# Optimization experiments

Hardware: AMD Instinct MI355X
Metric: run time of the kernel (lower is better)

## Reference

```python
import jax, jax.numpy as jnp
import numpy as np

RES = 64  # fixed roi_map resolution (replaces per-ROI ceil(width)/ceil(height) dynamic sizes for jit)
SMOOTH_L1_BETA = 1.0 / 9.0


def setup_inputs() -> dict:
    key = jax.random.key(0)
    ks = jax.random.split(key, 8)
    N, C = 4096, 91
    R, K, HM = 1024, 17, 56
    class_logits = jax.random.normal(ks[0], (N, C), dtype=jnp.float32)
    box_regression = jax.random.normal(ks[1], (N, C * 4), dtype=jnp.float32)
    labels = jax.random.randint(ks[2], (N,), 0, C, dtype=jnp.int32)
    regression_targets = jax.random.normal(ks[3], (N, 4), dtype=jnp.float32)
    kp_maps = jax.random.normal(ks[4], (R, K, HM, HM), dtype=jnp.float32)
    xy = jax.random.uniform(ks[5], (R, 2), dtype=jnp.float32) * 512.0
    wh = 32.0 + jax.random.uniform(ks[6], (R, 2), dtype=jnp.float32) * 256.0
    kp_rois = jnp.concatenate([xy, xy + wh], axis=1)  # valid xyxy boxes
    mask_logits = jax.random.normal(ks[7], (R, C, 28, 28), dtype=jnp.float32)
    mask_labels = jax.random.randint(jax.random.fold_in(key, 9), (R,), 0, C, dtype=jnp.int32)
    return {
        "class_logits": class_logits,
        "box_regression": box_regression,
        "labels": labels,
        "regression_targets": regression_targets,
        "kp_maps": kp_maps,
        "kp_rois": kp_rois,
        "mask_logits": mask_logits,
        "mask_labels": mask_labels,
    }


def _fastrcnn_loss(class_logits, box_regression, labels, regression_targets):
    N, C = class_logits.shape
    # classification: mean cross entropy
    logp = jax.nn.log_softmax(class_logits, axis=-1)
    cls_loss = -jnp.take_along_axis(logp, labels[:, None], axis=1)[:, 0].mean()
    br = box_regression.reshape(N, C, 4)
    sel = jnp.take_along_axis(br, labels[:, None, None].astype(jnp.int32) * jnp.ones((1, 1, 4), jnp.int32), axis=1)[:, 0]  # [N,4]
    d = sel - regression_targets
    ad = jnp.abs(d)
    sl1 = jnp.where(ad < SMOOTH_L1_BETA, 0.5 * d * d / SMOOTH_L1_BETA, ad - 0.5 * SMOOTH_L1_BETA)
    pos = (labels > 0).astype(sl1.dtype)
    box_loss = (sl1.sum(-1) * pos).sum() / N
    return cls_loss, box_loss


def _heatmaps_to_keypoints(maps, rois):
    # maps: [R,K,H,W], rois: [R,4] xyxy
    R, K, H, W = maps.shape
    offset_x, offset_y = rois[:, 0], rois[:, 1]
    widths = jnp.clip(rois[:, 2] - rois[:, 0], 1.0, None)
    heights = jnp.clip(rois[:, 3] - rois[:, 1], 1.0, None)
    width_corr = widths / RES   # [R]
    height_corr = heights / RES
    roi_map = jax.image.resize(maps, (R, K, RES, RES), method='bicubic')
    flat = roi_map.reshape(R, K, RES * RES)
    pos = jnp.argmax(flat, axis=-1)           # [R,K]
    x_int = pos % RES
    y_int = pos // RES
    x = (x_int.astype(jnp.float32) + 0.5) * width_corr[:, None] + offset_x[:, None]
    y = (y_int.astype(jnp.float32) + 0.5) * height_corr[:, None] + offset_y[:, None]
    xy_preds = jnp.stack([x, y, jnp.ones_like(x)], axis=-1)  # [R,K,3]
    end_scores = jnp.take_along_axis(flat, pos[..., None], axis=-1)[..., 0]  # [R,K]
    return xy_preds, end_scores


def _maskrcnn_inference(mask_logits, mask_labels):
    R = mask_logits.shape[0]
    probs = jax.nn.sigmoid(mask_logits)
    return probs[jnp.arange(R), mask_labels][:, None]  # [R,1,M,M]


def reference(class_logits, box_regression, labels, regression_targets,
              kp_maps, kp_rois, mask_logits, mask_labels):
    cls_loss, box_loss = _fastrcnn_loss(class_logits, box_regression, labels, regression_targets)
    xy_preds, end_scores = _heatmaps_to_keypoints(kp_maps, kp_rois)
    mask_prob = _maskrcnn_inference(mask_logits, mask_labels)
    return (cls_loss, box_loss, xy_preds, end_scores, mask_prob)
```

## Files before the change

### kernel.cpp

```cpp
#include <hip/hip_runtime.h>
#include <math.h>

#define RES 64
#define IN_HW 56
#define K_KP 17
#define N_ROWS 4096
#define N_CLS 91
#define R_ROIS 1024
#define SMOOTH_BETA (1.0f / 9.0f)


__device__ __forceinline__ float keys_cubic(float x) {
    x = fabsf(x);
    if (x < 1.f) return ((1.5f * x - 2.5f) * x) * x + 1.f;
    if (x < 2.f) return ((-0.5f * x + 2.5f) * x - 4.f) * x + 2.f;
    return 0.f;
}

__device__ __forceinline__ int fl_of(int o) { return (7 * o - 1) >> 3; }

__global__ __launch_bounds__(256) void loss_kernel(
    const float* __restrict__ logits, const float* __restrict__ boxreg,
    const int* __restrict__ labels, const float* __restrict__ tgt,
    float* __restrict__ out)
{
    __shared__ float s_cls[4], s_box[4];
    const int tid = threadIdx.x, wv = tid >> 6, ln = tid & 63;
    const int row = blockIdx.x * 4 + wv;

    const float* lr = logits + (size_t)row * N_CLS;
    float a = (ln < N_CLS) ? lr[ln] : -INFINITY;
    float b = (ln + 64 < N_CLS) ? lr[ln + 64] : -INFINITY;
    float m = fmaxf(a, b);
    #pragma unroll
    for (int off = 32; off; off >>= 1) m = fmaxf(m, __shfl_down(m, off));
    m = __shfl(m, 0);
    float e = 0.f;
    if (ln < N_CLS) e += expf(a - m);
    if (ln + 64 < N_CLS) e += expf(b - m);
    #pragma unroll
    for (int off = 32; off; off >>= 1) e += __shfl_down(e, off);
    if (ln == 0) {
        float lsm = m + logf(e);
        int lbl = labels[row];
        const float* sel = boxreg + (size_t)row * (4 * N_CLS) + lbl * 4;
        const float* tg = tgt + (size_t)row * 4;
        float s = 0.f;
        #pragma unroll
        for (int j = 0; j < 4; ++j) {
            float d = sel[j] - tg[j];
            float ad = fabsf(d);
            s += (ad < SMOOTH_BETA) ? (0.5f * d * d / SMOOTH_BETA)
                                    : (ad - 0.5f * SMOOTH_BETA);
        }
        s_cls[wv] = lsm - lr[lbl];
        s_box[wv] = (lbl > 0) ? s : 0.f;
    }
    __syncthreads();
    if (tid == 0) {
        float c = s_cls[0] + s_cls[1] + s_cls[2] + s_cls[3];
        float bx = s_box[0] + s_box[1] + s_box[2] + s_box[3];
        atomicAdd(&out[0], c * (1.f / (float)N_ROWS));
        atomicAdd(&out[1], bx * (1.f / (float)N_ROWS));
    }
}

__global__ __launch_bounds__(256) void kp_kernel(
    const float* __restrict__ maps, const float* __restrict__ rois,
    float* __restrict__ out)
{
    __shared__ float  sm_in[IN_HW * IN_HW];
    __shared__ float  sm_tmp[IN_HW * RES];
    __shared__ float4 s_w4[RES];
    __shared__ float  s_red_v[4];
    __shared__ int    s_red_i[4];

    const int map_id = blockIdx.x;
    const int tid = threadIdx.x;

    {
        const float4* src = (const float4*)(maps + (size_t)map_id * (IN_HW * IN_HW));
        float4* dst = (float4*)sm_in;
        for (int i = tid; i < (IN_HW * IN_HW) / 4; i += 256) dst[i] = src[i];
    }

    if (tid < RES) {
        float s = (tid + 0.5f) * (56.f / 64.f) - 0.5f;
        int fl = (int)floorf(s);
        float w[4]; float ws = 0.f;
        #pragma unroll
        for (int t = 0; t < 4; ++t) {
            int i = fl - 1 + t;
            float wv = keys_cubic(s - (float)i);
            if (i < 0 || i >= IN_HW) wv = 0.f;
            w[t] = wv; ws += wv;
        }
        float inv = 1.f / ws;
        s_w4[tid] = make_float4(w[0] * inv, w[1] * inv, w[2] * inv, w[3] * inv);
    }
    __syncthreads();

    {
        const int ox = tid & 63;
        const int fl = fl_of(ox);
        const int i0 = max(fl - 1, 0);
        const int i1 = max(fl, 0);
        const int i2 = min(fl + 1, IN_HW - 1);
        const int i3 = min(fl + 2, IN_HW - 1);
        const float4 w = s_w4[ox];
        for (int y = tid >> 6; y < IN_HW; y += 4) {
            const float* row = sm_in + y * IN_HW;
            sm_tmp[y * RES + ox] = w.x * row[i0] + w.y * row[i1]
                                 + w.z * row[i2] + w.w * row[i3];
        }
    }
    __syncthreads();

    float best = -INFINITY; int bidx = 0;
    {
        const int ox = tid & 63;
        const int oy0 = (tid >> 6) * 16;
        int fl = fl_of(oy0);
        #define CLAMP_ROW(i) (min(max((i), 0), IN_HW - 1))
        float r0 = sm_tmp[CLAMP_ROW(fl - 1) * RES + ox];
        float r1 = sm_tmp[CLAMP_ROW(fl    ) * RES + ox];
        float r2 = sm_tmp[CLAMP_ROW(fl + 1) * RES + ox];
        float r3 = sm_tmp[CLAMP_ROW(fl + 2) * RES + ox];
        #pragma unroll
        for (int k = 0; k < 16; ++k) {
            const int oy = oy0 + k;
            const float4 w = s_w4[oy];
            float v = w.x * r0 + w.y * r1 + w.z * r2 + w.w * r3;
            if (v > best) { best = v; bidx = oy * RES + ox; }
            if (k < 15) {
                int nfl = fl_of(oy + 1);
                if (nfl != fl) {
                    r0 = r1; r1 = r2; r2 = r3;
                    r3 = sm_tmp[CLAMP_ROW(nfl + 2) * RES + ox];
                    fl = nfl;
                }
            }
        }
        #undef CLAMP_ROW
    }
    #pragma unroll
    for (int off = 32; off; off >>= 1) {
        float ov = __shfl_down(best, off);
        int   oi = __shfl_down(bidx, off);
        if (ov > best || (ov == best && oi < bidx)) { best = ov; bidx = oi; }
    }
    const int wv = tid >> 6, ln = tid & 63;
    if (ln == 0) { s_red_v[wv] = best; s_red_i[wv] = bidx; }
    __syncthreads();
    if (tid == 0) {
        float bv = s_red_v[0]; int bi = s_red_i[0];
        #pragma unroll
        for (int w = 1; w < 4; ++w) {
            float v = s_red_v[w]; int i2 = s_red_i[w];
            if (v > bv || (v == bv && i2 < bi)) { bv = v; bi = i2; }
        }
        const int r = map_id / K_KP;
        const float x0 = rois[r * 4 + 0], y0r = rois[r * 4 + 1];
        const float x1 = rois[r * 4 + 2], y1r = rois[r * 4 + 3];
        const float wdt = fmaxf(x1 - x0, 1.f), hgt = fmaxf(y1r - y0r, 1.f);
        const float wc = wdt * (1.f / 64.f), hc = hgt * (1.f / 64.f);
        const int xi = bi & 63, yi = bi >> 6;
        float* xyp = out + 2 + (size_t)map_id * 3;
        xyp[0] = ((float)xi + 0.5f) * wc + x0;
        xyp[1] = ((float)yi + 0.5f) * hc + y0r;
        xyp[2] = 1.f;
        out[52226 + map_id] = bv;
    }
}

__global__ __launch_bounds__(256) void mask_kernel(
    const float* __restrict__ ml, const int* __restrict__ mlab,
    float* __restrict__ out)
{
    const int r = blockIdx.x, tid = threadIdx.x;
    const int lbl = mlab[r];
    const float2* src = (const float2*)(ml + ((size_t)r * N_CLS + lbl) * 784);
    float2* dst = (float2*)(out + 69634 + (size_t)r * 784);
    for (int i = tid; i < 392; i += 256) {
        float2 v = src[i];
        float2 o;
        o.x = 1.f / (1.f + expf(-v.x));
        o.y = 1.f / (1.f + expf(-v.y));
        dst[i] = o;
    }
}

extern "C" void kernel_launch(void* const* d_in, const int* in_sizes, int n_in,
                              void* d_out, int out_size, void* d_ws, size_t ws_size,
                              hipStream_t stream) {
    const float* class_logits = (const float*)d_in[0];
    const float* box_regression = (const float*)d_in[1];
    const int*   labels = (const int*)d_in[2];
    const float* regression_targets = (const float*)d_in[3];
    const float* kp_maps = (const float*)d_in[4];
    const float* kp_rois = (const float*)d_in[5];
    const float* mask_logits = (const float*)d_in[6];
    const int*   mask_labels = (const int*)d_in[7];
    float* out = (float*)d_out;

    hipMemsetAsync(d_out, 0, 2 * sizeof(float), stream);

    loss_kernel<<<N_ROWS / 4, 256, 0, stream>>>(class_logits, box_regression,
                                                labels, regression_targets, out);
    kp_kernel<<<R_ROIS * K_KP, 256, 0, stream>>>(kp_maps, kp_rois, out);
    mask_kernel<<<R_ROIS, 256, 0, stream>>>(mask_logits, mask_labels, out);
}
```

Baseline: 539.1 us.

## Fuse loss, keypoint and mask kernels into one launch with deterministic reduction

Merges the three separate kernels into one grid that dispatches on block index: keypoint blocks first, then loss blocks, then mask blocks. The memset and per-block atomics are replaced by per-block partial sums written to workspace and a small finishing kernel. The aim is to cut launch overhead and the tail gaps between kernels, and to let the short loss and mask blocks fill the machine alongside the keypoint blocks. In exchange the loss and mask blocks now carry the keypoint kernel's shared-memory footprint, and a second launch is still required.

```diff
diff --git a/kernel.cpp b/kernel.cpp
--- a/kernel.cpp
+++ b/kernel.cpp
@@ -9,6 +9,11 @@
 #define R_ROIS 1024
 #define SMOOTH_BETA (1.0f / 9.0f)
 
+#define KP_BLOCKS (R_ROIS * K_KP)
+#define LOSS_BLOCKS 256
+#define MASK_START (KP_BLOCKS + LOSS_BLOCKS)
+#define TOTAL_BLOCKS (MASK_START + R_ROIS)
+
 
 __device__ __forceinline__ float keys_cubic(float x) {
     x = fabsf(x);
@@ -19,55 +24,12 @@
 
 __device__ __forceinline__ int fl_of(int o) { return (7 * o - 1) >> 3; }
 
-__global__ __launch_bounds__(256) void loss_kernel(
+__global__ __launch_bounds__(256) void fused_kernel(
+    const float* __restrict__ maps, const float* __restrict__ rois,
     const float* __restrict__ logits, const float* __restrict__ boxreg,
     const int* __restrict__ labels, const float* __restrict__ tgt,
-    float* __restrict__ out)
-{
-    __shared__ float s_cls[4], s_box[4];
-    const int tid = threadIdx.x, wv = tid >> 6, ln = tid & 63;
-    const int row = blockIdx.x * 4 + wv;
-
-    const float* lr = logits + (size_t)row * N_CLS;
-    float a = (ln < N_CLS) ? lr[ln] : -INFINITY;
-    float b = (ln + 64 < N_CLS) ? lr[ln + 64] : -INFINITY;
-    float m = fmaxf(a, b);
-    #pragma unroll
-    for (int off = 32; off; off >>= 1) m = fmaxf(m, __shfl_down(m, off));
-    m = __shfl(m, 0);
-    float e = 0.f;
-    if (ln < N_CLS) e += expf(a - m);
-    if (ln + 64 < N_CLS) e += expf(b - m);
-    #pragma unroll
-    for (int off = 32; off; off >>= 1) e += __shfl_down(e, off);
-    if (ln == 0) {
-        float lsm = m + logf(e);
-        int lbl = labels[row];
-        const float* sel = boxreg + (size_t)row * (4 * N_CLS) + lbl * 4;
-        const float* tg = tgt + (size_t)row * 4;
-        float s = 0.f;
-        #pragma unroll
-        for (int j = 0; j < 4; ++j) {
-            float d = sel[j] - tg[j];
-            float ad = fabsf(d);
-            s += (ad < SMOOTH_BETA) ? (0.5f * d * d / SMOOTH_BETA)
-                                    : (ad - 0.5f * SMOOTH_BETA);
-        }
-        s_cls[wv] = lsm - lr[lbl];
-        s_box[wv] = (lbl > 0) ? s : 0.f;
-    }
-    __syncthreads();
-    if (tid == 0) {
-        float c = s_cls[0] + s_cls[1] + s_cls[2] + s_cls[3];
-        float bx = s_box[0] + s_box[1] + s_box[2] + s_box[3];
-        atomicAdd(&out[0], c * (1.f / (float)N_ROWS));
-        atomicAdd(&out[1], bx * (1.f / (float)N_ROWS));
-    }
-}
-
-__global__ __launch_bounds__(256) void kp_kernel(
-    const float* __restrict__ maps, const float* __restrict__ rois,
-    float* __restrict__ out)
+    const float* __restrict__ ml, const int* __restrict__ mlab,
+    float* __restrict__ out, float* __restrict__ ws)
 {
     __shared__ float  sm_in[IN_HW * IN_HW];
     __shared__ float  sm_tmp[IN_HW * RES];
@@ -75,118 +37,187 @@
     __shared__ float  s_red_v[4];
     __shared__ int    s_red_i[4];
 
-    const int map_id = blockIdx.x;
+    const int bid = blockIdx.x;
     const int tid = threadIdx.x;
-
-    {
-        const float4* src = (const float4*)(maps + (size_t)map_id * (IN_HW * IN_HW));
-        float4* dst = (float4*)sm_in;
-        for (int i = tid; i < (IN_HW * IN_HW) / 4; i += 256) dst[i] = src[i];
-    }
-
-    if (tid < RES) {
-        float s = (tid + 0.5f) * (56.f / 64.f) - 0.5f;
-        int fl = (int)floorf(s);
-        float w[4]; float ws = 0.f;
+    const int wv = tid >> 6, ln = tid & 63;
+
+    if (bid < KP_BLOCKS) {
+        const int map_id = bid;
+
+        {
+            const float4* src = (const float4*)(maps + (size_t)map_id * (IN_HW * IN_HW));
+            float4* dst = (float4*)sm_in;
+            for (int i = tid; i < (IN_HW * IN_HW) / 4; i += 256) dst[i] = src[i];
+        }
+
+        if (tid < RES) {
+            float s = (tid + 0.5f) * (56.f / 64.f) - 0.5f;
+            int fl = (int)floorf(s);
+            float w[4]; float wsum = 0.f;
+            #pragma unroll
+            for (int t = 0; t < 4; ++t) {
+                int i = fl - 1 + t;
+                float wv2 = keys_cubic(s - (float)i);
+                if (i < 0 || i >= IN_HW) wv2 = 0.f;
+                w[t] = wv2; wsum += wv2;
+            }
+            float inv = 1.f / wsum;
+            s_w4[tid] = make_float4(w[0] * inv, w[1] * inv, w[2] * inv, w[3] * inv);
+        }
+        __syncthreads();
+
+        {
+            const int ox = ln;
+            const int fl = fl_of(ox);
+            const int i0 = max(fl - 1, 0);
+            const int i1 = max(fl, 0);
+            const int i2 = min(fl + 1, IN_HW - 1);
+            const int i3 = min(fl + 2, IN_HW - 1);
+            const float4 w = s_w4[ox];
+            for (int y = wv; y < IN_HW; y += 4) {
+                const float* row = sm_in + y * IN_HW;
+                sm_tmp[y * RES + ox] = w.x * row[i0] + w.y * row[i1]
+                                     + w.z * row[i2] + w.w * row[i3];
+            }
+        }
+        __syncthreads();
+
+        float best = -INFINITY; int bidx = 0;
+        {
+            const int ox = ln;
+            const int oy0 = wv * 16;
+            int fl = fl_of(oy0);
+            #define CLAMP_ROW(i) (min(max((i), 0), IN_HW - 1))
+            float r0 = sm_tmp[CLAMP_ROW(fl - 1) * RES + ox];
+            float r1 = sm_tmp[CLAMP_ROW(fl    ) * RES + ox];
+            float r2 = sm_tmp[CLAMP_ROW(fl + 1) * RES + ox];
+            float r3 = sm_tmp[CLAMP_ROW(fl + 2) * RES + ox];
+            #pragma unroll
+            for (int k = 0; k < 16; ++k) {
+                const int oy = oy0 + k;
+                const float4 w = s_w4[oy];
+                float v = w.x * r0 + w.y * r1 + w.z * r2 + w.w * r3;
+                if (v > best) { best = v; bidx = oy * RES + ox; }
+                if (k < 15) {
+                    int nfl = fl_of(oy + 1);
+                    if (nfl != fl) {
+                        r0 = r1; r1 = r2; r2 = r3;
+                        r3 = sm_tmp[CLAMP_ROW(nfl + 2) * RES + ox];
+                        fl = nfl;
+                    }
+                }
+            }
+            #undef CLAMP_ROW
+        }
         #pragma unroll
-        for (int t = 0; t < 4; ++t) {
-            int i = fl - 1 + t;
-            float wv = keys_cubic(s - (float)i);
-            if (i < 0 || i >= IN_HW) wv = 0.f;
-            w[t] = wv; ws += wv;
-        }
-        float inv = 1.f / ws;
-        s_w4[tid] = make_float4(w[0] * inv, w[1] * inv, w[2] * inv, w[3] * inv);
-    }
+        for (int off = 32; off; off >>= 1) {
+            float ov = __shfl_down(best, off);
+            int   oi = __shfl_down(bidx, off);
+            if (ov > best || (ov == best && oi < bidx)) { best = ov; bidx = oi; }
+        }
+        if (ln == 0) { s_red_v[wv] = best; s_red_i[wv] = bidx; }
+        __syncthreads();
+        if (tid == 0) {
+            float bv = s_red_v[0]; int bi = s_red_i[0];
+            #pragma unroll
+            for (int w = 1; w < 4; ++w) {
+                float v = s_red_v[w]; int i2 = s_red_i[w];
+                if (v > bv || (v == bv && i2 < bi)) { bv = v; bi = i2; }
+            }
+            const int r = map_id / K_KP;
+            const float x0 = rois[r * 4 + 0], y0r = rois[r * 4 + 1];
+            const float x1 = rois[r * 4 + 2], y1r = rois[r * 4 + 3];
+            const float wdt = fmaxf(x1 - x0, 1.f), hgt = fmaxf(y1r - y0r, 1.f);
+            const float wc = wdt * (1.f / 64.f), hc = hgt * (1.f / 64.f);
+            const int xi = bi & 63, yi = bi >> 6;
+            float* xyp = out + 2 + (size_t)map_id * 3;
+            xyp[0] = ((float)xi + 0.5f) * wc + x0;
+            xyp[1] = ((float)yi + 0.5f) * hc + y0r;
+            xyp[2] = 1.f;
+            out[52226 + map_id] = bv;
+        }
+        return;
+    }
+
+    if (bid >= MASK_START) {
+        const int r = bid - MASK_START;
+        const int lbl = mlab[r];
+        const float2* src = (const float2*)(ml + ((size_t)r * N_CLS + lbl) * 784);
+        float2* dst = (float2*)(out + 69634 + (size_t)r * 784);
+        for (int i = tid; i < 392; i += 256) {
+            float2 v = src[i];
+            float2 o;
+            o.x = 1.f / (1.f + expf(-v.x));
+            o.y = 1.f / (1.f + expf(-v.y));
+            dst[i] = o;
+        }
+        return;
+    }
+
+    const int b = bid - KP_BLOCKS;
+    float csum = 0.f, bsum = 0.f;
+    #pragma unroll
+    for (int i = 0; i < 4; ++i) {
+        const int row = b * 16 + wv * 4 + i;
+        const float* lr = logits + (size_t)row * N_CLS;
+        float a  = (ln < N_CLS) ? lr[ln] : -INFINITY;
+        float a2 = (ln + 64 < N_CLS) ? lr[ln + 64] : -INFINITY;
+        float m = fmaxf(a, a2);
+        #pragma unroll
+        for (int off = 32; off; off >>= 1) m = fmaxf(m, __shfl_down(m, off));
+        m = __shfl(m, 0);
+        float e = 0.f;
+        if (ln < N_CLS) e += expf(a - m);
+        if (ln + 64 < N_CLS) e += expf(a2 - m);
+        #pragma unroll
+        for (int off = 32; off; off >>= 1) e += __shfl_down(e, off);
+        if (ln == 0) {
+            float lsm = m + logf(e);
+            int lbl = labels[row];
+            const float* sel = boxreg + (size_t)row * (4 * N_CLS) + lbl * 4;
+            const float* tg = tgt + (size_t)row * 4;
+            float s = 0.f;
+            #pragma unroll
+            for (int j = 0; j < 4; ++j) {
+                float d = sel[j] - tg[j];
+                float ad = fabsf(d);
+                s += (ad < SMOOTH_BETA) ? (0.5f * d * d / SMOOTH_BETA)
+                                        : (ad - 0.5f * SMOOTH_BETA);
+            }
+            csum += lsm - lr[lbl];
+            if (lbl > 0) bsum += s;
+        }
+    }
+    if (ln == 0) { s_red_v[wv] = csum; s_red_i[wv] = __float_as_int(bsum); }
     __syncthreads();
-
-    {
-        const int ox = tid & 63;
-        const int fl = fl_of(ox);
-        const int i0 = max(fl - 1, 0);
-        const int i1 = max(fl, 0);
-        const int i2 = min(fl + 1, IN_HW - 1);
-        const int i3 = min(fl + 2, IN_HW - 1);
-        const float4 w = s_w4[ox];
-        for (int y = tid >> 6; y < IN_HW; y += 4) {
-            const float* row = sm_in + y * IN_HW;
-            sm_tmp[y * RES + ox] = w.x * row[i0] + w.y * row[i1]
-                                 + w.z * row[i2] + w.w * row[i3];
-        }
-    }
-    __syncthreads();
-
-    float best = -INFINITY; int bidx = 0;
-    {
-        const int ox = tid & 63;
-        const int oy0 = (tid >> 6) * 16;
-        int fl = fl_of(oy0);
-        #define CLAMP_ROW(i) (min(max((i), 0), IN_HW - 1))
-        float r0 = sm_tmp[CLAMP_ROW(fl - 1) * RES + ox];
-        float r1 = sm_tmp[CLAMP_ROW(fl    ) * RES + ox];
-        float r2 = sm_tmp[CLAMP_ROW(fl + 1) * RES + ox];
-        float r3 = sm_tmp[CLAMP_ROW(fl + 2) * RES + ox];
-        #pragma unroll
-        for (int k = 0; k < 16; ++k) {
-            const int oy = oy0 + k;
-            const float4 w = s_w4[oy];
-            float v = w.x * r0 + w.y * r1 + w.z * r2 + w.w * r3;
-            if (v > best) { best = v; bidx = oy * RES + ox; }
-            if (k < 15) {
-                int nfl = fl_of(oy + 1);
-                if (nfl != fl) {
-                    r0 = r1; r1 = r2; r2 = r3;
-                    r3 = sm_tmp[CLAMP_ROW(nfl + 2) * RES + ox];
-                    fl = nfl;
-                }
-            }
-        }
-        #undef CLAMP_ROW
-    }
+    if (tid == 0) {
+        float c  = s_red_v[0] + s_red_v[1] + s_red_v[2] + s_red_v[3];
+        float bx = __int_as_float(s_red_i[0]) + __int_as_float(s_red_i[1])
+                 + __int_as_float(s_red_i[2]) + __int_as_float(s_red_i[3]);
+        ws[b * 2]     = c;
+        ws[b * 2 + 1] = bx;
+    }
+}
+
+__global__ __launch_bounds__(256) void loss_finish(
+    const float* __restrict__ ws, float* __restrict__ out)
+{
+    __shared__ float s_c[4], s_b[4];
+    const int tid = threadIdx.x, wv = tid >> 6, ln = tid & 63;
+    float c = ws[tid * 2];
+    float b = ws[tid * 2 + 1];
     #pragma unroll
     for (int off = 32; off; off >>= 1) {
-        float ov = __shfl_down(best, off);
-        int   oi = __shfl_down(bidx, off);
-        if (ov > best || (ov == best && oi < bidx)) { best = ov; bidx = oi; }
-    }
-    const int wv = tid >> 6, ln = tid & 63;
-    if (ln == 0) { s_red_v[wv] = best; s_red_i[wv] = bidx; }
+        c += __shfl_down(c, off);
+        b += __shfl_down(b, off);
+    }
+    if (ln == 0) { s_c[wv] = c; s_b[wv] = b; }
     __syncthreads();
     if (tid == 0) {
-        float bv = s_red_v[0]; int bi = s_red_i[0];
-        #pragma unroll
-        for (int w = 1; w < 4; ++w) {
-            float v = s_red_v[w]; int i2 = s_red_i[w];
-            if (v > bv || (v == bv && i2 < bi)) { bv = v; bi = i2; }
-        }
-        const int r = map_id / K_KP;
-        const float x0 = rois[r * 4 + 0], y0r = rois[r * 4 + 1];
-        const float x1 = rois[r * 4 + 2], y1r = rois[r * 4 + 3];
-        const float wdt = fmaxf(x1 - x0, 1.f), hgt = fmaxf(y1r - y0r, 1.f);
-        const float wc = wdt * (1.f / 64.f), hc = hgt * (1.f / 64.f);
-        const int xi = bi & 63, yi = bi >> 6;
-        float* xyp = out + 2 + (size_t)map_id * 3;
-        xyp[0] = ((float)xi + 0.5f) * wc + x0;
-        xyp[1] = ((float)yi + 0.5f) * hc + y0r;
-        xyp[2] = 1.f;
-        out[52226 + map_id] = bv;
-    }
-}
-
-__global__ __launch_bounds__(256) void mask_kernel(
-    const float* __restrict__ ml, const int* __restrict__ mlab,
-    float* __restrict__ out)
-{
-    const int r = blockIdx.x, tid = threadIdx.x;
-    const int lbl = mlab[r];
-    const float2* src = (const float2*)(ml + ((size_t)r * N_CLS + lbl) * 784);
-    float2* dst = (float2*)(out + 69634 + (size_t)r * 784);
-    for (int i = tid; i < 392; i += 256) {
-        float2 v = src[i];
-        float2 o;
-        o.x = 1.f / (1.f + expf(-v.x));
-        o.y = 1.f / (1.f + expf(-v.y));
-        dst[i] = o;
+        float cc = s_c[0] + s_c[1] + s_c[2] + s_c[3];
+        float bb = s_b[0] + s_b[1] + s_b[2] + s_b[3];
+        out[0] = cc * (1.f / (float)N_ROWS);
+        out[1] = bb * (1.f / (float)N_ROWS);
     }
 }
 
@@ -202,11 +233,10 @@
     const float* mask_logits = (const float*)d_in[6];
     const int*   mask_labels = (const int*)d_in[7];
     float* out = (float*)d_out;
-
-    hipMemsetAsync(d_out, 0, 2 * sizeof(float), stream);
-
-    loss_kernel<<<N_ROWS / 4, 256, 0, stream>>>(class_logits, box_regression,
-                                                labels, regression_targets, out);
-    kp_kernel<<<R_ROIS * K_KP, 256, 0, stream>>>(kp_maps, kp_rois, out);
-    mask_kernel<<<R_ROIS, 256, 0, stream>>>(mask_logits, mask_labels, out);
-}
+    float* ws  = (float*)d_ws;
+
+    fused_kernel<<<TOTAL_BLOCKS, 256, 0, stream>>>(
+        kp_maps, kp_rois, class_logits, box_regression, labels,
+        regression_targets, mask_logits, mask_labels, out, ws);
+    loss_finish<<<1, 256, 0, stream>>>(ws, out);
+}
```

Result: faster. 512.2 us (-5.0%).
